# Kernel tuning notes

Measured on AMD Instinct MI355X. Metric: run time of the kernel, lower is better.

## Reference

```python
import jax, jax.numpy as jnp
import numpy as np

H, D = 4, 32          # heads, per-head dim (= hidden_channels)
HD = H * D            # concat width fed between layers
L = 2                 # num HGT layers
OUT = 128             # final output dim
SCALE = 1.0 / np.sqrt(D)


def _seg_softmax(score, seg, n):
    # segment softmax over incoming edges per destination node, per head
    mx = jax.ops.segment_max(score, seg, num_segments=n)
    ex = jnp.exp(score - mx[seg])
    den = jax.ops.segment_sum(ex, seg, num_segments=n)
    return ex / den[seg]


def _hgt_side(q_dst, k_src, v_src, src, dst, a_rel, m_rel, p_rel, n_dst):
    # k/v: [N_src,H,D]; a_rel,m_rel: [H,D,D]; p_rel: [H]
    k_t = jnp.einsum('ehd,hdf->ehf', k_src[src], a_rel)          # [E,H,D]
    score = (q_dst[dst] * k_t).sum(-1) * p_rel * SCALE           # [E,H]
    alpha = _seg_softmax(score, dst, n_dst)                      # [E,H]
    v_t = jnp.einsum('ehd,hdf->ehf', v_src[src], m_rel)          # [E,H,D]
    return jax.ops.segment_sum(alpha[..., None] * v_t, dst, num_segments=n_dst)


def _forward(x_m, x_g, W_in_m, b_in_m, W_in_g, b_in_g,
             Wk_m, bk_m, Wq_m, bq_m, Wv_m, bv_m,
             Wk_g, bk_g, Wq_g, bq_g, Wv_g, bv_g,
             a_mg, m_mg, p_mg, a_gm, m_gm, p_gm,
             Wa_m, ba_m, Wa_g, ba_g, skip_m, skip_g,
             W_out_m, b_out_m, W_out_g, b_out_g,
             edge_mg_src, edge_mg_dst, edge_gm_src, edge_gm_dst):
    Nm, Ng = x_m.shape[0], x_g.shape[0]
    # per-node-type input projection
    h_m = x_m @ W_in_m + b_in_m                                  # [Nm,HD]
    h_g = x_g @ W_in_g + b_in_g                                  # [Ng,HD]
    for l in range(L):
        k_m = (h_m @ Wk_m[l] + bk_m[l]).reshape(Nm, H, D)
        q_m = (h_m @ Wq_m[l] + bq_m[l]).reshape(Nm, H, D)
        v_m = (h_m @ Wv_m[l] + bv_m[l]).reshape(Nm, H, D)
        k_g = (h_g @ Wk_g[l] + bk_g[l]).reshape(Ng, H, D)
        q_g = (h_g @ Wq_g[l] + bq_g[l]).reshape(Ng, H, D)
        v_g = (h_g @ Wv_g[l] + bv_g[l]).reshape(Ng, H, D)
        agg_g = _hgt_side(q_g, k_m, v_m, edge_mg_src, edge_mg_dst,
                          a_mg[l], m_mg[l], p_mg[l], Ng)         # [Ng,H,D]
        agg_m = _hgt_side(q_m, k_g, v_g, edge_gm_src, edge_gm_dst,
                          a_gm[l], m_gm[l], p_gm[l], Nm)         # [Nm,H,D]
        o_m = jax.nn.gelu(agg_m.reshape(Nm, HD), approximate=False) @ Wa_m[l] + ba_m[l]
        o_g = jax.nn.gelu(agg_g.reshape(Ng, HD), approximate=False) @ Wa_g[l] + ba_g[l]
        bm = jax.nn.sigmoid(skip_m[l])
        bg = jax.nn.sigmoid(skip_g[l])
        h_m = jax.nn.elu(bm * o_m + (1.0 - bm) * h_m)            # HGTConv skip, then model-level ELU
        h_g = jax.nn.elu(bg * o_g + (1.0 - bg) * h_g)
    out_m = h_m @ W_out_m + b_out_m                              # [Nm,OUT]
    out_g = h_g @ W_out_g + b_out_g                              # [Ng,OUT]
    return jnp.concatenate([out_m, out_g], axis=0)               # [Nm+Ng,OUT]


def setup_inputs() -> dict:
    key = jax.random.key(0)
    ks = iter(jax.random.split(key, 64))
    Nm, Ng, E = 100000, 20000, 500000
    Fm, Fg = 20, 50
    def n(shape, s=0.05):
        return jax.random.normal(next(ks), shape, jnp.float32) * s
    inp = {
        'x_m': n((Nm, Fm), 1.0), 'x_g': n((Ng, Fg), 1.0),
        'W_in_m': n((Fm, HD)), 'b_in_m': jnp.zeros((HD,), jnp.float32),
        'W_in_g': n((Fg, HD)), 'b_in_g': jnp.zeros((HD,), jnp.float32),
        'Wk_m': n((L, HD, HD)), 'bk_m': jnp.zeros((L, HD), jnp.float32),
        'Wq_m': n((L, HD, HD)), 'bq_m': jnp.zeros((L, HD), jnp.float32),
        'Wv_m': n((L, HD, HD)), 'bv_m': jnp.zeros((L, HD), jnp.float32),
        'Wk_g': n((L, HD, HD)), 'bk_g': jnp.zeros((L, HD), jnp.float32),
        'Wq_g': n((L, HD, HD)), 'bq_g': jnp.zeros((L, HD), jnp.float32),
        'Wv_g': n((L, HD, HD)), 'bv_g': jnp.zeros((L, HD), jnp.float32),
        'a_mg': n((L, H, D, D)), 'm_mg': n((L, H, D, D)),
        'p_mg': jnp.ones((L, H), jnp.float32),
        'a_gm': n((L, H, D, D)), 'm_gm': n((L, H, D, D)),
        'p_gm': jnp.ones((L, H), jnp.float32),
        'Wa_m': n((L, HD, HD)), 'ba_m': jnp.zeros((L, HD), jnp.float32),
        'Wa_g': n((L, HD, HD)), 'ba_g': jnp.zeros((L, HD), jnp.float32),
        'skip_m': jnp.ones((L,), jnp.float32), 'skip_g': jnp.ones((L,), jnp.float32),
        'W_out_m': n((HD, OUT)), 'b_out_m': jnp.zeros((OUT,), jnp.float32),
        'W_out_g': n((HD, OUT)), 'b_out_g': jnp.zeros((OUT,), jnp.float32),
        'edge_mg_src': jax.random.randint(next(ks), (E,), 0, Nm, jnp.int32),
        'edge_mg_dst': jax.random.randint(next(ks), (E,), 0, Ng, jnp.int32),
        'edge_gm_src': jax.random.randint(next(ks), (E,), 0, Ng, jnp.int32),
        'edge_gm_dst': jax.random.randint(next(ks), (E,), 0, Nm, jnp.int32),
    }
    return inp


def reference(x_m, x_g, W_in_m, b_in_m, W_in_g, b_in_g,
              Wk_m, bk_m, Wq_m, bq_m, Wv_m, bv_m,
              Wk_g, bk_g, Wq_g, bq_g, Wv_g, bv_g,
              a_mg, m_mg, p_mg, a_gm, m_gm, p_gm,
              Wa_m, ba_m, Wa_g, ba_g, skip_m, skip_g,
              W_out_m, b_out_m, W_out_g, b_out_g,
              edge_mg_src, edge_mg_dst, edge_gm_src, edge_gm_dst):
    return _forward(x_m, x_g, W_in_m, b_in_m, W_in_g, b_in_g,
                    Wk_m, bk_m, Wq_m, bq_m, Wv_m, bv_m,
                    Wk_g, bk_g, Wq_g, bq_g, Wv_g, bv_g,
                    a_mg, m_mg, p_mg, a_gm, m_gm, p_gm,
                    Wa_m, ba_m, Wa_g, ba_g, skip_m, skip_g,
                    W_out_m, b_out_m, W_out_g, b_out_g,
                    edge_mg_src, edge_mg_dst, edge_gm_src, edge_gm_dst)
```

## Files before the change

### kernel.cpp

```cpp
#include <hip/hip_runtime.h>
#include <hip/hip_bf16.h>

#define SCALE_F 0.17677669529663688f

typedef __attribute__((ext_vector_type(8)))  short bfrag;
typedef __attribute__((ext_vector_type(16))) float facc;

__device__ __forceinline__ float lo16(unsigned u){ return __uint_as_float(u << 16); }
__device__ __forceinline__ float hi16(unsigned u){ return __uint_as_float(u & 0xffff0000u); }
__device__ __forceinline__ float bu2f(unsigned short u){ return __uint_as_float((unsigned)u << 16); }
__device__ __forceinline__ unsigned short f2bu(float f){
    __hip_bfloat16 h = __float2bfloat16(f);
    return *reinterpret_cast<unsigned short*>(&h);
}
__device__ __forceinline__ void storeC(float* p, float v){ *p = v; }
__device__ __forceinline__ void storeC(__hip_bfloat16* p, float v){ *p = __float2bfloat16(v); }
__device__ __forceinline__ void up8(uint4 v, float* f){
    f[0]=lo16(v.x); f[1]=hi16(v.x); f[2]=lo16(v.y); f[3]=hi16(v.y);
    f[4]=lo16(v.z); f[5]=hi16(v.z); f[6]=lo16(v.w); f[7]=hi16(v.w);
}

__global__ void hist_k(const int* __restrict__ dst, int* __restrict__ cnt, int E, int Nd){
    int e = blockIdx.x*256 + threadIdx.x;
    if (e >= E) return;
    int d = dst[e];
    if ((unsigned)d < (unsigned)Nd) atomicAdd(&cnt[d], 1);
}

__global__ void scan_block_k(const int* __restrict__ cnt, int* __restrict__ incl,
                             int* __restrict__ bsum, int N){
    __shared__ int sh[256];
    int tid = threadIdx.x;
    int i = blockIdx.x*256 + tid;
    int v = (i < N) ? cnt[i] : 0;
    sh[tid] = v;
    __syncthreads();
    for (int off = 1; off < 256; off <<= 1){
        int t = (tid >= off) ? sh[tid-off] : 0;
        __syncthreads();
        sh[tid] += t;
        __syncthreads();
    }
    if (i < N) incl[i] = sh[tid];
    if (tid == 255) bsum[blockIdx.x] = sh[255];
}

__global__ void scan_top_k(int* __restrict__ bsum, int nb){
    __shared__ int sh[512];
    int tid = threadIdx.x;
    int v = (tid < nb) ? bsum[tid] : 0;
    sh[tid] = v;
    __syncthreads();
    for (int off = 1; off < 512; off <<= 1){
        int t = (tid >= off) ? sh[tid-off] : 0;
        __syncthreads();
        sh[tid] += t;
        __syncthreads();
    }
    if (tid < nb) bsum[tid] = sh[tid] - v;
}

__global__ void finalize_k(const int* __restrict__ incl, const int* __restrict__ cnt,
                           const int* __restrict__ boff, int* __restrict__ indptr,
                           int N, int E){
    int i = blockIdx.x*256 + threadIdx.x;
    if (i > N) return;
    if (i == N){ indptr[N] = E; return; }
    indptr[i] = boff[i >> 8] + incl[i] - cnt[i];
}

__global__ void scatter_k(const int* __restrict__ src, const int* __restrict__ dst,
                          const int* __restrict__ indptr, int* __restrict__ cur,
                          int* __restrict__ csr, int E, int Nd){
    int e = blockIdx.x*256 + threadIdx.x;
    if (e >= E) return;
    int d = dst[e];
    if ((unsigned)d >= (unsigned)Nd) return;
    int p = indptr[d] + atomicAdd(&cur[d], 1);
    csr[p] = src[e];
}

template<int K>
__global__ __launch_bounds__(128) void in_proj_k(const float* __restrict__ x,
                                                 const float* __restrict__ W,
                                                 const float* __restrict__ b,
                                                 unsigned short* __restrict__ h, int N){
    constexpr int KP4 = (K + 3)/4, KP = KP4*4;
    int j = threadIdx.x;
    float wreg[KP];
    #pragma unroll
    for (int k = 0; k < KP; ++k) wreg[k] = (k < K) ? W[k*128 + j] : 0.f;
    float bj = b[j];
    __shared__ float xs[8][KP];
    for (int base = blockIdx.x*8; base < N; base += gridDim.x*8){
        __syncthreads();
        for (int t = threadIdx.x; t < 8*KP; t += 128){
            int r = t / KP, k = t - r*KP;
            int row = base + r;
            xs[r][k] = (row < N && k < K) ? x[(size_t)row*K + k] : 0.f;
        }
        __syncthreads();
        #pragma unroll
        for (int r = 0; r < 8; ++r){
            int row = base + r;
            if (row >= N) break;
            float acc = bj;
            #pragma unroll
            for (int kk = 0; kk < KP4; ++kk){
                float4 xv = *(const float4*)(&xs[r][kk*4]);
                acc += xv.x*wreg[kk*4] + xv.y*wreg[kk*4+1]
                     + xv.z*wreg[kk*4+2] + xv.w*wreg[kk*4+3];
            }
            h[(size_t)row*128 + j] = f2bu(acc);
        }
    }
}

__global__ __launch_bounds__(128) void build_wf2_k(
    const float* __restrict__ Wq0, const float* __restrict__ bq0,
    const float* __restrict__ Wk0, const float* __restrict__ bk0,
    const float* __restrict__ Wv0, const float* __restrict__ bv0,
    const float* __restrict__ ar0, const float* __restrict__ mr0,
    unsigned short* __restrict__ Wto0, float* __restrict__ bfo0,
    const float* __restrict__ Wq1, const float* __restrict__ bq1,
    const float* __restrict__ Wk1, const float* __restrict__ bk1,
    const float* __restrict__ Wv1, const float* __restrict__ bv1,
    const float* __restrict__ ar1, const float* __restrict__ mr1,
    unsigned short* __restrict__ Wto1, float* __restrict__ bfo1){
    bool sA = (blockIdx.y == 0);
    const float* Wq = sA ? Wq0 : Wq1;  const float* bq = sA ? bq0 : bq1;
    const float* Wk = sA ? Wk0 : Wk1;  const float* bk = sA ? bk0 : bk1;
    const float* Wv = sA ? Wv0 : Wv1;  const float* bvp = sA ? bv0 : bv1;
    const float* ar = sA ? ar0 : ar1;  const float* mr = sA ? mr0 : mr1;
    unsigned short* Wt = sA ? Wto0 : Wto1;
    float* bf = sA ? bfo0 : bfo1;
    int j = blockIdx.x, row = threadIdx.x;
    int part = j >> 7, f = j & 127, hh = f >> 5, ff = f & 31;
    float v;
    if (part == 0) v = Wq[row*128 + f];
    else {
        const float* Wx  = (part == 1) ? Wk : Wv;
        const float* rel = (part == 1) ? ar : mr;
        float s = 0.f;
        #pragma unroll
        for (int d = 0; d < 32; ++d)
            s += Wx[row*128 + hh*32 + d] * rel[hh*1024 + d*32 + ff];
        v = s;
    }
    Wt[(size_t)j*128 + row] = f2bu(v);
    if (row == 0){
        float bb;
        if (part == 0) bb = bq[f];
        else {
            const float* bx  = (part == 1) ? bk : bvp;
            const float* rel = (part == 1) ? ar : mr;
            float s = 0.f;
            for (int d = 0; d < 32; ++d)
                s += bx[hh*32 + d] * rel[hh*1024 + d*32 + ff];
            bb = s;
        }
        bf[j] = bb;
    }
}

__global__ void transpose6_k(const float* a0, const float* a1, const float* a2,
                             const float* a3, const float* a4, const float* a5,
                             unsigned short* d0, unsigned short* d1, unsigned short* d2,
                             unsigned short* d3, unsigned short* d4, unsigned short* d5){
    int y = blockIdx.y;
    const float* S = (y==0)?a0:(y==1)?a1:(y==2)?a2:(y==3)?a3:(y==4)?a4:a5;
    unsigned short* D = (y==0)?d0:(y==1)?d1:(y==2)?d2:(y==3)?d3:(y==4)?d4:d5;
    int idx = blockIdx.x*256 + threadIdx.x;
    int n = idx >> 7, k = idx & 127;
    D[idx] = f2bu(S[k*128 + n]);
}

template<typename CT, int MODE>
__global__ __launch_bounds__(256) void mfma_gemm2(
    const unsigned short* __restrict__ A0, const unsigned short* __restrict__ Wt0,
    const float* __restrict__ bias0, CT* __restrict__ C0, unsigned short* __restrict__ H0,
    int N0, const float* __restrict__ skip0,
    const unsigned short* __restrict__ A1, const unsigned short* __restrict__ Wt1,
    const float* __restrict__ bias1, CT* __restrict__ C1, unsigned short* __restrict__ H1,
    int N1, const float* __restrict__ skip1,
    int ldc, int nblk0){
    bool s0 = ((int)blockIdx.x < nblk0);
    const unsigned short* A  = s0 ? A0 : A1;
    const unsigned short* Wt = s0 ? Wt0 : Wt1;
    const float* bias = s0 ? bias0 : bias1;
    CT* C = s0 ? C0 : C1;
    unsigned short* H = s0 ? H0 : H1;
    int N = s0 ? N0 : N1;
    const float* skip = s0 ? skip0 : skip1;
    int bx = s0 ? blockIdx.x : (blockIdx.x - nblk0);

    __shared__ unsigned short As[64][136];
    __shared__ unsigned short Bs[128][136];
    int tid = threadIdx.x;
    int rb = bx*64, cb = blockIdx.y*128;
    #pragma unroll
    for (int ph = 0; ph < 4; ++ph){
        int c = ph*256 + tid;
        int r = c >> 4, off = (c & 15)*8;
        uint4 v = make_uint4(0,0,0,0);
        if (rb + r < N) v = ((const uint4*)(A + (size_t)(rb + r)*128))[c & 15];
        *(uint4*)(&As[r][off]) = v;
    }
    #pragma unroll
    for (int ph = 0; ph < 8; ++ph){
        int c = ph*256 + tid;
        int r = c >> 4, off = (c & 15)*8;
        uint4 v = ((const uint4*)(Wt + (size_t)(cb + r)*128))[c & 15];
        *(uint4*)(&Bs[r][off]) = v;
    }
    __syncthreads();
    int w = tid >> 6, lane = tid & 63;
    int wr = (w >> 1)*32, wc = (w & 1)*64;
    int m = lane & 31, quad = lane >> 5;
    facc acc0, acc1;
    #pragma unroll
    for (int i = 0; i < 16; ++i){ acc0[i] = 0.f; acc1[i] = 0.f; }
    const unsigned short* ap  = &As[wr + m][quad*8];
    const unsigned short* bp0 = &Bs[wc + m][quad*8];
    const unsigned short* bp1 = &Bs[wc + 32 + m][quad*8];
    #pragma unroll
    for (int kc = 0; kc < 8; ++kc){
        bfrag a  = *(const bfrag*)(ap  + kc*16);
        bfrag b0 = *(const bfrag*)(bp0 + kc*16);
        bfrag b1 = *(const bfrag*)(bp1 + kc*16);
        acc0 = __builtin_amdgcn_mfma_f32_32x32x16_bf16(a, b0, acc0, 0, 0, 0);
        acc1 = __builtin_amdgcn_mfma_f32_32x32x16_bf16(a, b1, acc1, 0, 0, 0);
    }
    int col0 = cb + wc + m, col1 = col0 + 32;
    float bias0v = bias[col0], bias1v = bias[col1];
    float bm = 0.f;
    if (MODE == 2) bm = 1.f/(1.f + __expf(-skip[0]));
    #pragma unroll
    for (int r = 0; r < 16; ++r){
        int lrow = wr + 4*quad + (r & 3) + 8*(r >> 2);
        int grow = rb + lrow;
        if (grow >= N) continue;
        float o0 = acc0[r] + bias0v;
        float o1 = acc1[r] + bias1v;
        if (MODE == 0){
            storeC(&C[(size_t)grow*ldc + col0], o0);
            storeC(&C[(size_t)grow*ldc + col1], o1);
        } else {
            size_t i0 = (size_t)grow*128 + col0, i1 = (size_t)grow*128 + col1;
            float v0 = bm*o0 + (1.f - bm)*bu2f(H[i0]);
            float v1 = bm*o1 + (1.f - bm)*bu2f(H[i1]);
            v0 = (v0 > 0.f) ? v0 : expm1f(v0);
            v1 = (v1 > 0.f) ? v1 : expm1f(v1);
            H[i0] = f2bu(v0);
            H[i1] = f2bu(v1);
        }
    }
}

__global__ __launch_bounds__(256) void edge_attn3_k(
    const int* __restrict__ ipA, const int* __restrict__ csrA,
    const unsigned short* __restrict__ qdA, const unsigned short* __restrict__ qsA,
    const float* __restrict__ pA, unsigned* __restrict__ aggA, int NdA,
    const int* __restrict__ ipB, const int* __restrict__ csrB,
    const unsigned short* __restrict__ qdB, const unsigned short* __restrict__ qsB,
    const float* __restrict__ pB, unsigned* __restrict__ aggB, int NdB,
    int nblkA){
    bool sA = ((int)blockIdx.x < nblkA);
    const int* ip  = sA ? ipA : ipB;
    const int* csr = sA ? csrA : csrB;
    const unsigned* qd = (const unsigned*)(sA ? qdA : qdB);
    const unsigned* qs = (const unsigned*)(sA ? qsA : qsB);
    const float* p = sA ? pA : pB;
    unsigned* agg = sA ? aggA : aggB;
    int Nd = sA ? NdA : NdB;
    int bx = sA ? blockIdx.x : (blockIdx.x - nblkA);
    int wid  = (bx << 2) | (threadIdx.x >> 6);
    int lane = threadIdx.x & 63;
    if (wid >= Nd) return;
    int slot = lane >> 4, j = lane & 15;
    float ph = p[j >> 2] * SCALE_F;
    uint4 qv = ((const uint4*)(qd + (size_t)wid*192))[j];
    float q[8]; up8(qv, q);
    int beg = ip[wid], end = ip[wid + 1];
    float den = 0.f;
    float acc[8] = {0.f,0.f,0.f,0.f,0.f,0.f,0.f,0.f};
    for (int i = beg + slot; i < end; i += 4){
        int s = csr[i];
        const uint4* base = (const uint4*)(qs + (size_t)s*192);
        uint4 kv = base[16 + j];
        uint4 vv = base[32 + j];
        float kf[8]; up8(kv, kf);
        float part = q[0]*kf[0] + q[1]*kf[1] + q[2]*kf[2] + q[3]*kf[3]
                   + q[4]*kf[4] + q[5]*kf[5] + q[6]*kf[6] + q[7]*kf[7];
        part += __shfl_xor(part, 1);
        part += __shfl_xor(part, 2);
        float e = __expf(part * ph);
        float vf[8]; up8(vv, vf);
        den += e;
        #pragma unroll
        for (int d = 0; d < 8; ++d) acc[d] += e * vf[d];
    }
    den += __shfl_xor(den, 16);
    den += __shfl_xor(den, 32);
    #pragma unroll
    for (int d = 0; d < 8; ++d){
        acc[d] += __shfl_xor(acc[d], 16);
        acc[d] += __shfl_xor(acc[d], 32);
    }
    float inv = (den > 0.f) ? 1.f/den : 0.f;
    float o0 = acc[2*slot]*inv, o1 = acc[2*slot + 1]*inv;
    o0 = 0.5f*o0*(1.f + erff(o0*0.70710678118654752f));
    o1 = 0.5f*o1*(1.f + erff(o1*0.70710678118654752f));
    agg[(size_t)wid*64 + j*4 + slot] = (unsigned)f2bu(o0) | ((unsigned)f2bu(o1) << 16);
}

extern "C" void kernel_launch(void* const* d_in, const int* in_sizes, int n_in,
                              void* d_out, int out_size, void* d_ws, size_t ws_size,
                              hipStream_t stream){
    typedef const float* FP;
    FP x_m = (FP)d_in[0], x_g = (FP)d_in[1];
    FP W_in_m = (FP)d_in[2], b_in_m = (FP)d_in[3], W_in_g = (FP)d_in[4], b_in_g = (FP)d_in[5];
    FP Wk_m = (FP)d_in[6],  bk_m = (FP)d_in[7],  Wq_m = (FP)d_in[8],  bq_m = (FP)d_in[9];
    FP Wv_m = (FP)d_in[10], bv_m = (FP)d_in[11];
    FP Wk_g = (FP)d_in[12], bk_g = (FP)d_in[13], Wq_g = (FP)d_in[14], bq_g = (FP)d_in[15];
    FP Wv_g = (FP)d_in[16], bv_g = (FP)d_in[17];
    FP a_mg = (FP)d_in[18], m_mg = (FP)d_in[19], p_mg = (FP)d_in[20];
    FP a_gm = (FP)d_in[21], m_gm = (FP)d_in[22], p_gm = (FP)d_in[23];
    FP Wa_m = (FP)d_in[24], ba_m = (FP)d_in[25], Wa_g = (FP)d_in[26], ba_g = (FP)d_in[27];
    FP skip_m = (FP)d_in[28], skip_g = (FP)d_in[29];
    FP W_out_m = (FP)d_in[30], b_out_m = (FP)d_in[31], W_out_g = (FP)d_in[32], b_out_g = (FP)d_in[33];
    const int* e_mg_src = (const int*)d_in[34];
    const int* e_mg_dst = (const int*)d_in[35];
    const int* e_gm_src = (const int*)d_in[36];
    const int* e_gm_dst = (const int*)d_in[37];

    const int Nm = in_sizes[0] / 20;
    const int Ng = in_sizes[1] / 50;
    const int E1 = in_sizes[34];
    const int E2 = in_sizes[36];

    char* wp = (char*)d_ws;
    auto alloc = [&](size_t bytes) -> char* {
        char* r = wp; wp += (bytes + 255) & ~(size_t)255; return r;
    };
    unsigned short* h_m   = (unsigned short*)alloc((size_t)Nm*128*2);
    unsigned short* h_g   = (unsigned short*)alloc((size_t)Ng*128*2);
    unsigned short* agg_m = (unsigned short*)alloc((size_t)Nm*128*2);
    unsigned short* agg_g = (unsigned short*)alloc((size_t)Ng*128*2);
    unsigned short* qkv_m = (unsigned short*)alloc((size_t)Nm*384*2);
    unsigned short* qkv_g = (unsigned short*)alloc((size_t)Ng*384*2);
    unsigned short* Wtf   = (unsigned short*)alloc((size_t)4*49152*2);
    float*          bfv   = (float*)alloc((size_t)4*384*4);
    unsigned short* Wta   = (unsigned short*)alloc((size_t)4*16384*2);
    unsigned short* Wtout = (unsigned short*)alloc((size_t)2*16384*2);
    int* indptr_g = (int*)alloc((size_t)(Ng+1)*4);
    int* csr_mg   = (int*)alloc((size_t)E1*4);
    int* indptr_m = (int*)alloc((size_t)(Nm+1)*4);
    int* csr_gm   = (int*)alloc((size_t)E2*4);
    int maxN = Nm > Ng ? Nm : Ng;
    int* cnt  = (int*)alloc((size_t)maxN*4);
    int* cur  = (int*)alloc((size_t)maxN*4);
    int* cnt2 = (int*)alloc((size_t)maxN*4);
    int* cur2 = (int*)alloc((size_t)maxN*4);
    int* incl = (int*)alloc((size_t)maxN*4);
    int* bsum = (int*)alloc(512*4);

    size_t used = (size_t)(wp - (char*)d_ws);
    if (used > ws_size){
        hipMemsetAsync(d_out, 0, (size_t)out_size*4, stream);
        return;
    }
    hipMemsetAsync(cnt, 0, (size_t)((char*)cur2 - (char*)cnt) + (size_t)maxN*4, stream);

    auto buildCSR = [&](const int* esrc, const int* edst, int E, int Nd,
                        int* indptr, int* csr, int* c0, int* c1){
        hist_k<<<(E + 255)/256, 256, 0, stream>>>(edst, c0, E, Nd);
        int nb = (Nd + 255)/256;
        scan_block_k<<<nb, 256, 0, stream>>>(c0, incl, bsum, Nd);
        scan_top_k<<<1, 512, 0, stream>>>(bsum, nb);
        finalize_k<<<(Nd + 256)/256 + 1, 256, 0, stream>>>(incl, c0, bsum, indptr, Nd, E);
        scatter_k<<<(E + 255)/256, 256, 0, stream>>>(esrc, edst, indptr, c1, csr, E, Nd);
    };
    buildCSR(e_mg_src, e_mg_dst, E1, Ng, indptr_g, csr_mg, cnt, cur);
    buildCSR(e_gm_src, e_gm_dst, E2, Nm, indptr_m, csr_gm, cnt2, cur2);

    transpose6_k<<<dim3(64, 6), 256, 0, stream>>>(
        Wa_m, Wa_g, Wa_m + 16384, Wa_g + 16384, W_out_m, W_out_g,
        Wta, Wta + 16384, Wta + 32768, Wta + 49152, Wtout, Wtout + 16384);
    for (int l = 0; l < 2; ++l){
        build_wf2_k<<<dim3(384, 2), 128, 0, stream>>>(
            Wq_m + l*16384, bq_m + l*128, Wk_m + l*16384, bk_m + l*128,
            Wv_m + l*16384, bv_m + l*128, a_mg + l*4096, m_mg + l*4096,
            Wtf + (size_t)(l*2+0)*49152, bfv + (l*2+0)*384,
            Wq_g + l*16384, bq_g + l*128, Wk_g + l*16384, bk_g + l*128,
            Wv_g + l*16384, bv_g + l*128, a_gm + l*4096, m_gm + l*4096,
            Wtf + (size_t)(l*2+1)*49152, bfv + (l*2+1)*384);
    }

    int gim = (Nm + 7)/8; if (gim > 2048) gim = 2048;
    int gig = (Ng + 7)/8; if (gig > 2048) gig = 2048;
    in_proj_k<20><<<gim, 128, 0, stream>>>(x_m, W_in_m, b_in_m, h_m, Nm);
    in_proj_k<50><<<gig, 128, 0, stream>>>(x_g, W_in_g, b_in_g, h_g, Ng);

    int gxm = (Nm + 63)/64, gxg = (Ng + 63)/64;
    int nbA = (Ng + 3)/4, nbB = (Nm + 3)/4;

    for (int l = 0; l < 2; ++l){
        mfma_gemm2<__hip_bfloat16, 0><<<dim3(gxm + gxg, 3), 256, 0, stream>>>(
            h_m, Wtf + (size_t)(l*2+0)*49152, bfv + (l*2+0)*384,
            (__hip_bfloat16*)qkv_m, nullptr, Nm, nullptr,
            h_g, Wtf + (size_t)(l*2+1)*49152, bfv + (l*2+1)*384,
            (__hip_bfloat16*)qkv_g, nullptr, Ng, nullptr,
            384, gxm);

        edge_attn3_k<<<nbA + nbB, 256, 0, stream>>>(
            indptr_g, csr_mg, qkv_g, qkv_m, p_mg + l*4, (unsigned*)agg_g, Ng,
            indptr_m, csr_gm, qkv_m, qkv_g, p_gm + l*4, (unsigned*)agg_m, Nm,
            nbA);

        mfma_gemm2<float, 2><<<dim3(gxm + gxg, 1), 256, 0, stream>>>(
            agg_m, Wta + (size_t)(l*2+0)*16384, ba_m + l*128, (float*)nullptr, h_m, Nm, skip_m + l,
            agg_g, Wta + (size_t)(l*2+1)*16384, ba_g + l*128, (float*)nullptr, h_g, Ng, skip_g + l,
            128, gxm);
    }

    float* outp = (float*)d_out;
    mfma_gemm2<float, 0><<<dim3(gxm + gxg, 1), 256, 0, stream>>>(
        h_m, Wtout, b_out_m, outp, nullptr, Nm, nullptr,
        h_g, Wtout + 16384, b_out_g, outp + (size_t)Nm*128, nullptr, Ng, nullptr,
        128, gxm);
}
```

Before: 644.8 us.

## Batch both CSR builds into paired launches and prefetch next edge in attention

The two per-relation CSR construction pipelines (histogram, block scan, top scan, finalize, scatter) are merged into single launches using blockIdx.y to select the relation, halving the number of small kernel launches. Separate incl/bsum buffers are allocated so both relations can be scanned at once. The edge attention loop is software-pipelined to load the next neighbor's K/V rows before computing on the current one, hiding gather latency at the cost of extra registers.

```diff
diff --git a/kernel.cpp b/kernel.cpp
--- a/kernel.cpp
+++ b/kernel.cpp
@@ -20,15 +20,25 @@
     f[4]=lo16(v.z); f[5]=hi16(v.z); f[6]=lo16(v.w); f[7]=hi16(v.w);
 }
 
-__global__ void hist_k(const int* __restrict__ dst, int* __restrict__ cnt, int E, int Nd){
+__global__ void hist2_k(const int* __restrict__ d1, int* __restrict__ c1, int E1, int N1,
+                        const int* __restrict__ d2, int* __restrict__ c2, int E2, int N2){
+    const int* d = blockIdx.y ? d2 : d1;
+    int* c = blockIdx.y ? c2 : c1;
+    int E = blockIdx.y ? E2 : E1;
+    int Nd = blockIdx.y ? N2 : N1;
     int e = blockIdx.x*256 + threadIdx.x;
     if (e >= E) return;
-    int d = dst[e];
-    if ((unsigned)d < (unsigned)Nd) atomicAdd(&cnt[d], 1);
-}
-
-__global__ void scan_block_k(const int* __restrict__ cnt, int* __restrict__ incl,
-                             int* __restrict__ bsum, int N){
+    int dd = d[e];
+    if ((unsigned)dd < (unsigned)Nd) atomicAdd(&c[dd], 1);
+}
+
+__global__ void scan_block2_k(const int* __restrict__ c1, int* __restrict__ i1, int* __restrict__ b1, int N1,
+                              const int* __restrict__ c2, int* __restrict__ i2, int* __restrict__ b2, int N2){
+    const int* cnt = blockIdx.y ? c2 : c1;
+    int* incl = blockIdx.y ? i2 : i1;
+    int* bsum = blockIdx.y ? b2 : b1;
+    int N = blockIdx.y ? N2 : N1;
+    if ((int)blockIdx.x*256 >= N) return;
     __shared__ int sh[256];
     int tid = threadIdx.x;
     int i = blockIdx.x*256 + tid;
@@ -45,7 +55,9 @@
     if (tid == 255) bsum[blockIdx.x] = sh[255];
 }
 
-__global__ void scan_top_k(int* __restrict__ bsum, int nb){
+__global__ void scan_top2_k(int* __restrict__ b1, int nb1, int* __restrict__ b2, int nb2){
+    int* bsum = blockIdx.x ? b2 : b1;
+    int nb = blockIdx.x ? nb2 : nb1;
     __shared__ int sh[512];
     int tid = threadIdx.x;
     int v = (tid < nb) ? bsum[tid] : 0;
@@ -60,18 +72,35 @@
     if (tid < nb) bsum[tid] = sh[tid] - v;
 }
 
-__global__ void finalize_k(const int* __restrict__ incl, const int* __restrict__ cnt,
-                           const int* __restrict__ boff, int* __restrict__ indptr,
-                           int N, int E){
+__global__ void finalize2_k(const int* __restrict__ i1, const int* __restrict__ c1,
+                            const int* __restrict__ b1, int* __restrict__ p1, int N1, int E1,
+                            const int* __restrict__ i2, const int* __restrict__ c2,
+                            const int* __restrict__ b2, int* __restrict__ p2, int N2, int E2){
+    const int* incl = blockIdx.y ? i2 : i1;
+    const int* cnt  = blockIdx.y ? c2 : c1;
+    const int* boff = blockIdx.y ? b2 : b1;
+    int* indptr = blockIdx.y ? p2 : p1;
+    int N = blockIdx.y ? N2 : N1;
+    int E = blockIdx.y ? E2 : E1;
     int i = blockIdx.x*256 + threadIdx.x;
     if (i > N) return;
     if (i == N){ indptr[N] = E; return; }
     indptr[i] = boff[i >> 8] + incl[i] - cnt[i];
 }
 
-__global__ void scatter_k(const int* __restrict__ src, const int* __restrict__ dst,
-                          const int* __restrict__ indptr, int* __restrict__ cur,
-                          int* __restrict__ csr, int E, int Nd){
+__global__ void scatter2_k(const int* __restrict__ s1, const int* __restrict__ d1,
+                           const int* __restrict__ p1, int* __restrict__ u1,
+                           int* __restrict__ r1, int E1, int N1,
+                           const int* __restrict__ s2, const int* __restrict__ d2,
+                           const int* __restrict__ p2, int* __restrict__ u2,
+                           int* __restrict__ r2, int E2, int N2){
+    const int* src = blockIdx.y ? s2 : s1;
+    const int* dst = blockIdx.y ? d2 : d1;
+    const int* indptr = blockIdx.y ? p2 : p1;
+    int* cur = blockIdx.y ? u2 : u1;
+    int* csr = blockIdx.y ? r2 : r1;
+    int E = blockIdx.y ? E2 : E1;
+    int Nd = blockIdx.y ? N2 : N1;
     int e = blockIdx.x*256 + threadIdx.x;
     if (e >= E) return;
     int d = dst[e];
@@ -257,7 +286,7 @@
     }
 }
 
-__global__ __launch_bounds__(256) void edge_attn3_k(
+__global__ __launch_bounds__(256) void edge_attn4_k(
     const int* __restrict__ ipA, const int* __restrict__ csrA,
     const unsigned short* __restrict__ qdA, const unsigned short* __restrict__ qsA,
     const float* __restrict__ pA, unsigned* __restrict__ aggA, int NdA,
@@ -284,21 +313,35 @@
     int beg = ip[wid], end = ip[wid + 1];
     float den = 0.f;
     float acc[8] = {0.f,0.f,0.f,0.f,0.f,0.f,0.f,0.f};
-    for (int i = beg + slot; i < end; i += 4){
+    int i = beg + slot;
+    if (i < end){
         int s = csr[i];
-        const uint4* base = (const uint4*)(qs + (size_t)s*192);
-        uint4 kv = base[16 + j];
-        uint4 vv = base[32 + j];
-        float kf[8]; up8(kv, kf);
-        float part = q[0]*kf[0] + q[1]*kf[1] + q[2]*kf[2] + q[3]*kf[3]
-                   + q[4]*kf[4] + q[5]*kf[5] + q[6]*kf[6] + q[7]*kf[7];
-        part += __shfl_xor(part, 1);
-        part += __shfl_xor(part, 2);
-        float e = __expf(part * ph);
-        float vf[8]; up8(vv, vf);
-        den += e;
-        #pragma unroll
-        for (int d = 0; d < 8; ++d) acc[d] += e * vf[d];
+        const uint4* b = (const uint4*)(qs + (size_t)s*192);
+        uint4 kv = b[16 + j];
+        uint4 vv = b[32 + j];
+        while (true){
+            int inx = i + 4;
+            bool more = (inx < end);
+            uint4 kv2, vv2;
+            if (more){
+                int s2 = csr[inx];
+                const uint4* b2 = (const uint4*)(qs + (size_t)s2*192);
+                kv2 = b2[16 + j];
+                vv2 = b2[32 + j];
+            }
+            float kf[8]; up8(kv, kf);
+            float part = q[0]*kf[0] + q[1]*kf[1] + q[2]*kf[2] + q[3]*kf[3]
+                       + q[4]*kf[4] + q[5]*kf[5] + q[6]*kf[6] + q[7]*kf[7];
+            part += __shfl_xor(part, 1);
+            part += __shfl_xor(part, 2);
+            float e = __expf(part * ph);
+            float vf[8]; up8(vv, vf);
+            den += e;
+            #pragma unroll
+            for (int d = 0; d < 8; ++d) acc[d] += e * vf[d];
+            if (!more) break;
+            i = inx; kv = kv2; vv = vv2;
+        }
     }
     den += __shfl_xor(den, 16);
     den += __shfl_xor(den, 32);
@@ -363,7 +406,9 @@
     int* cnt2 = (int*)alloc((size_t)maxN*4);
     int* cur2 = (int*)alloc((size_t)maxN*4);
     int* incl = (int*)alloc((size_t)maxN*4);
+    int* incl2= (int*)alloc((size_t)maxN*4);
     int* bsum = (int*)alloc(512*4);
+    int* bsum2= (int*)alloc(512*4);
 
     size_t used = (size_t)(wp - (char*)d_ws);
     if (used > ws_size){
@@ -372,17 +417,19 @@
     }
     hipMemsetAsync(cnt, 0, (size_t)((char*)cur2 - (char*)cnt) + (size_t)maxN*4, stream);
 
-    auto buildCSR = [&](const int* esrc, const int* edst, int E, int Nd,
-                        int* indptr, int* csr, int* c0, int* c1){
-        hist_k<<<(E + 255)/256, 256, 0, stream>>>(edst, c0, E, Nd);
-        int nb = (Nd + 255)/256;
-        scan_block_k<<<nb, 256, 0, stream>>>(c0, incl, bsum, Nd);
-        scan_top_k<<<1, 512, 0, stream>>>(bsum, nb);
-        finalize_k<<<(Nd + 256)/256 + 1, 256, 0, stream>>>(incl, c0, bsum, indptr, Nd, E);
-        scatter_k<<<(E + 255)/256, 256, 0, stream>>>(esrc, edst, indptr, c1, csr, E, Nd);
-    };
-    buildCSR(e_mg_src, e_mg_dst, E1, Ng, indptr_g, csr_mg, cnt, cur);
-    buildCSR(e_gm_src, e_gm_dst, E2, Nm, indptr_m, csr_gm, cnt2, cur2);
+    int maxE = E1 > E2 ? E1 : E2;
+    int nb1 = (Ng + 255)/256, nb2 = (Nm + 255)/256;
+    int nbmax = nb1 > nb2 ? nb1 : nb2;
+    hist2_k<<<dim3((maxE + 255)/256, 2), 256, 0, stream>>>(
+        e_mg_dst, cnt, E1, Ng, e_gm_dst, cnt2, E2, Nm);
+    scan_block2_k<<<dim3(nbmax, 2), 256, 0, stream>>>(
+        cnt, incl, bsum, Ng, cnt2, incl2, bsum2, Nm);
+    scan_top2_k<<<2, 512, 0, stream>>>(bsum, nb1, bsum2, nb2);
+    finalize2_k<<<dim3(nbmax + 1, 2), 256, 0, stream>>>(
+        incl, cnt, bsum, indptr_g, Ng, E1, incl2, cnt2, bsum2, indptr_m, Nm, E2);
+    scatter2_k<<<dim3((maxE + 255)/256, 2), 256, 0, stream>>>(
+        e_mg_src, e_mg_dst, indptr_g, cur, csr_mg, E1, Ng,
+        e_gm_src, e_gm_dst, indptr_m, cur2, csr_gm, E2, Nm);
 
     transpose6_k<<<dim3(64, 6), 256, 0, stream>>>(
         Wa_m, Wa_g, Wa_m + 16384, Wa_g + 16384, W_out_m, W_out_g,
@@ -413,7 +460,7 @@
             (__hip_bfloat16*)qkv_g, nullptr, Ng, nullptr,
             384, gxm);
 
-        edge_attn3_k<<<nbA + nbB, 256, 0, stream>>>(
+        edge_attn4_k<<<nbA + nbB, 256, 0, stream>>>(
             indptr_g, csr_mg, qkv_g, qkv_m, p_mg + l*4, (unsigned*)agg_g, Ng,
             indptr_m, csr_gm, qkv_m, qkv_g, p_gm + l*4, (unsigned*)agg_m, Nm,
             nbA);
```

After: 617.0 us. 1.05x faster.
